# Kernel optimization log

Measured on AMD Instinct MI355X. Metric: run time of the kernel, lower is better.

## Reference

```python
import jax, jax.numpy as jnp
import numpy as np

MODEL_DIM = 1024
NUM_HEADS = 16
CHUNK_LEN = 2048
HEAD_DIM = MODEL_DIM // NUM_HEADS


def setup_inputs() -> dict:
    key = jax.random.key(0)
    ks = jax.random.split(key, 11)
    s = 1.0 / np.sqrt(MODEL_DIM)
    inp = {
        "Q": jax.random.normal(ks[0], (CHUNK_LEN, MODEL_DIM), dtype=jnp.float32),
        "K": jax.random.normal(ks[1], (CHUNK_LEN, MODEL_DIM), dtype=jnp.float32),
        "V": jax.random.normal(ks[2], (CHUNK_LEN, MODEL_DIM), dtype=jnp.float32),
        "Wq": jax.random.normal(ks[3], (MODEL_DIM, MODEL_DIM), dtype=jnp.float32) * s,
        "bq": jax.random.normal(ks[4], (MODEL_DIM,), dtype=jnp.float32) * s,
        "Wk": jax.random.normal(ks[5], (MODEL_DIM, MODEL_DIM), dtype=jnp.float32) * s,
        "bk": jax.random.normal(ks[6], (MODEL_DIM,), dtype=jnp.float32) * s,
        "Wv": jax.random.normal(ks[7], (MODEL_DIM, MODEL_DIM), dtype=jnp.float32) * s,
        "bv": jax.random.normal(ks[8], (MODEL_DIM,), dtype=jnp.float32) * s,
        "Wo": jax.random.normal(ks[9], (MODEL_DIM, MODEL_DIM), dtype=jnp.float32) * s,
        "bo": jax.random.normal(ks[10], (MODEL_DIM,), dtype=jnp.float32) * s,
    }
    return inp


def reference(Q, K, V, Wq, bq, Wk, bk, Wv, bv, Wo, bo):
    S = CHUNK_LEN
    # Linear projections (equinox Linear: y = W @ x + b, vmapped over tokens)
    q = Q @ Wq.T + bq  # [S, D]
    k = K @ Wk.T + bk
    v = V @ Wv.T + bv
    # split heads -> [H, S, hd]
    q = q.reshape(S, NUM_HEADS, HEAD_DIM).transpose(1, 0, 2)
    k = k.reshape(S, NUM_HEADS, HEAD_DIM).transpose(1, 0, 2)
    v = v.reshape(S, NUM_HEADS, HEAD_DIM).transpose(1, 0, 2)
    # scaled dot-product attention with causal mask
    scores = jnp.einsum("hqd,hkd->hqk", q, k) / jnp.sqrt(
        jnp.asarray(HEAD_DIM, dtype=q.dtype)
    )  # [H, S, S]
    causal = jnp.tril(jnp.ones((S, S), dtype=bool))
    scores = jnp.where(causal, scores, -jnp.inf)
    probs = jax.nn.softmax(scores, axis=-1)
    attn = jnp.einsum("hqk,hkd->hqd", probs, v)  # [H, S, hd]
    # combine heads -> [S, D], output projection
    out = attn.transpose(1, 0, 2).reshape(S, MODEL_DIM)
    return out @ Wo.T + bo
```

## Files before the change

kernel.cpp:

```cpp
#include <hip/hip_runtime.h>
#include <hip/hip_bf16.h>
#include <stdint.h>

#define S_LEN  2048
#define DMODEL 1024
#define NHEADS 16
#define HDIM   64
#define CHUNK  7
#define NCHUNK 46

typedef __attribute__((ext_vector_type(8))) _Float16 half8;
typedef __attribute__((ext_vector_type(4))) _Float16 half4;
typedef __attribute__((ext_vector_type(4))) float    f32x4;

struct AttnMap { int base[17]; };

struct CvtArgs {
    const float* src[7];
    _Float16*    dst[7];
    int          n[7];
};

__global__ __launch_bounds__(256) void cvt_kernel(CvtArgs a) {
    const int z = blockIdx.z;
    const float* __restrict__ src = a.src[z];
    _Float16* __restrict__ dst = a.dst[z];
    const int n = a.n[z];
    const int stride = gridDim.x * blockDim.x * 8;
    for (int i = (blockIdx.x * blockDim.x + threadIdx.x) * 8; i < n; i += stride) {
        float4 v0 = *(const float4*)(src + i);
        float4 v1 = *(const float4*)(src + i + 4);
        half8 o;
        o[0] = (_Float16)v0.x; o[1] = (_Float16)v0.y;
        o[2] = (_Float16)v0.z; o[3] = (_Float16)v0.w;
        o[4] = (_Float16)v1.x; o[5] = (_Float16)v1.y;
        o[6] = (_Float16)v1.z; o[7] = (_Float16)v1.w;
        *(half8*)(dst + i) = o;
    }
}

__device__ __forceinline__ void gload16(const _Float16* g, _Float16* l) {
    __builtin_amdgcn_global_load_lds(
        (__attribute__((address_space(1))) void*)const_cast<_Float16*>(g),
        (__attribute__((address_space(3))) void*)l, 16, 0, 0);
}

template<typename OT>
__device__ __forceinline__ void gemm_body(
    const _Float16* __restrict__ A,
    const _Float16* __restrict__ W,
    const float*    __restrict__ bias,
    OT* __restrict__ C, float scale, int bx, int by)
{
    __shared__ _Float16 As[128 * 64];
    __shared__ _Float16 Bs[64 * 64];
    const int tid  = threadIdx.x;
    const int lane = tid & 63, wid = tid >> 6;
    const int row0 = by * 128;
    const int col0 = bx * 64;
    const int wr = wid >> 1, wc = wid & 1;
    const int lr = lane & 15, lg = lane >> 4;
    const int sl = lane & 7;

    f32x4 acc[4][2];
#pragma unroll
    for (int i = 0; i < 4; i++)
#pragma unroll
        for (int j = 0; j < 2; j++) acc[i][j] = (f32x4)(0.0f);

    for (int k0 = 0; k0 < DMODEL; k0 += 64) {
#pragma unroll
        for (int r = 0; r < 4; r++) {
            const int base = r * 256 + wid * 64;
            const int row  = (base + lane) >> 3;
            gload16(A + (size_t)(row0 + row) * DMODEL + k0 + ((sl ^ (row & 7)) * 8),
                    As + (size_t)base * 8);
        }
#pragma unroll
        for (int r = 0; r < 2; r++) {
            const int base = r * 256 + wid * 64;
            const int row  = (base + lane) >> 3;
            gload16(W + (size_t)(col0 + row) * DMODEL + k0 + ((sl ^ (row & 7)) * 8),
                    Bs + (size_t)base * 8);
        }
        __syncthreads();
#pragma unroll
        for (int ks = 0; ks < 2; ks++) {
            half8 af[4], bf[2];
#pragma unroll
            for (int i = 0; i < 4; i++)
                af[i] = *(const half8*)(As + (wr * 64 + i * 16 + lr) * 64 + (((ks * 4 + lg) ^ (lr & 7)) * 8));
#pragma unroll
            for (int j = 0; j < 2; j++)
                bf[j] = *(const half8*)(Bs + (wc * 32 + j * 16 + lr) * 64 + (((ks * 4 + lg) ^ (lr & 7)) * 8));
            __builtin_amdgcn_s_setprio(1);
#pragma unroll
            for (int i = 0; i < 4; i++)
#pragma unroll
                for (int j = 0; j < 2; j++)
                    acc[i][j] = __builtin_amdgcn_mfma_f32_16x16x32_f16(af[i], bf[j], acc[i][j], 0, 0, 0);
            __builtin_amdgcn_s_setprio(0);
        }
        __syncthreads();
    }
#pragma unroll
    for (int i = 0; i < 4; i++)
#pragma unroll
        for (int j = 0; j < 2; j++) {
            const int row = row0 + wr * 64 + i * 16 + lg * 4;
            const int col = col0 + wc * 32 + j * 16 + lr;
            const float b = bias[col];
#pragma unroll
            for (int rj = 0; rj < 4; rj++) {
                float v = (acc[i][j][rj] + b) * scale;
                if constexpr (sizeof(OT) == 2)
                    C[(size_t)(row + rj) * DMODEL + col] = (OT)(_Float16)v;
                else
                    C[(size_t)(row + rj) * DMODEL + col] = v;
            }
        }
}

struct QKVArgs {
    const _Float16* A[3];
    const _Float16* W[3];
    const float*    bias[3];
    _Float16*       C[3];
    float           scale[3];
};

__global__ __launch_bounds__(256) void gemm_qkv(QKVArgs a) {
    const int nper = (int)gridDim.x >> 3;
    const int sid  = ((int)blockIdx.x & 7) * nper + ((int)blockIdx.x >> 3);
    const int z  = sid >> 8;
    const int r  = sid & 255;
    const int by = r >> 4, bx = r & 15;
    gemm_body<_Float16>(a.A[z], a.W[z], a.bias[z], a.C[z], a.scale[z], bx, by);
}

__global__ __launch_bounds__(256) void gemm_out_k(const _Float16* __restrict__ A,
                                                  const _Float16* __restrict__ W,
                                                  const float* __restrict__ bias,
                                                  float* __restrict__ C) {
    const int nper = (int)gridDim.x >> 3;
    const int sid  = ((int)blockIdx.x & 7) * nper + ((int)blockIdx.x >> 3);
    const int by = sid >> 4, bx = sid & 15;
    gemm_body<float>(A, W, bias, C, 1.0f, bx, by);
}

__global__ __launch_bounds__(256) void transpose_v(const _Float16* __restrict__ v,
                                                   _Float16* __restrict__ Vt) {
    __shared__ _Float16 t[64][72];
    const int s0 = blockIdx.x * 64;
    const int h  = blockIdx.y;
    const int tid = threadIdx.x;
#pragma unroll
    for (int r = 0; r < 2; r++) {
        const int g = r * 256 + tid;
        const int sr = g >> 3, c8 = (g & 7) * 8;
        *(half8*)(&t[sr][c8]) = *(const half8*)(v + (size_t)(s0 + sr) * DMODEL + h * HDIM + c8);
    }
    __syncthreads();
#pragma unroll
    for (int r = 0; r < 2; r++) {
        const int g = r * 256 + tid;
        const int d = g >> 3, c8 = (g & 7) * 8;
        half8 o;
#pragma unroll
        for (int j = 0; j < 8; j++) o[j] = t[c8 + j][d];
        *(half8*)(Vt + (size_t)(h * HDIM + d) * S_LEN + s0 + c8) = o;
    }
}

__global__ __launch_bounds__(512, 6) void attn_kernel(
    const _Float16* __restrict__ q,
    const _Float16* __restrict__ k,
    const _Float16* __restrict__ Vt,
    _Float16* __restrict__ Opart,
    float2* __restrict__ ml,
    AttnMap map)
{
    __shared__ _Float16 Kl[2][64 * 64];
    __shared__ _Float16 Vl[2][64 * 64];
    __shared__ _Float16 P[8][16][72];
    const int tid = threadIdx.x, lane = tid & 63, wid = tid >> 6;
    const int x = NCHUNK - 1 - (int)blockIdx.x;
    const int h = blockIdx.y;
    int qt = 0;
    while (map.base[qt + 1] <= x) qt++;
    const int c  = x - map.base[qt];
    const int q0 = qt * 128 + wid * 16;
    const int lr = lane & 15, lg = lane >> 4;
    const int srcb = lg * 20;

    const int r8 = lane >> 3, sl = lane & 7;
    const int ssw = (sl ^ r8) * 8;

    half8 qf[2];
#pragma unroll
    for (int ds = 0; ds < 2; ds++)
        qf[ds] = *(const half8*)(q + (size_t)(q0 + lr) * DMODEL + h * HDIM + ds * 32 + lg * 8);

    float m = -1e30f, lsum = 0.0f;
    f32x4 od[4];
#pragma unroll
    for (int dt = 0; dt < 4; dt++) od[dt] = (f32x4)(0.0f);

    const int T2 = 2 * (qt + 1);
    const int t0 = c * CHUNK;
    const int t1 = (T2 < t0 + CHUNK) ? T2 : (t0 + CHUNK);

    auto stage = [&](int b, int t) {
        const int kb = t * 64;
        gload16(k + (size_t)(kb + wid * 8 + r8) * DMODEL + h * HDIM + ssw,
                &Kl[b][wid * 8 * 64]);
        gload16(Vt + (size_t)(h * HDIM + wid * 8 + r8) * S_LEN + kb + ssw,
                &Vl[b][wid * 8 * 64]);
    };

    int cur = 0;
    stage(0, t0);
    __syncthreads();

    for (int t = t0; t < t1; t++) {
        if (t + 1 < t1) stage(cur ^ 1, t + 1);
        const int k0 = t * 64;
        f32x4 sc[4];
#pragma unroll
        for (int kt = 0; kt < 4; kt++) sc[kt] = (f32x4)(0.0f);
        __builtin_amdgcn_s_setprio(1);
#pragma unroll
        for (int kt = 0; kt < 4; kt++)
#pragma unroll
            for (int ds = 0; ds < 2; ds++) {
                half8 kf = *(const half8*)(&Kl[cur][(kt * 16 + lr) * 64 + (((ds * 4 + lg) ^ (lr & 7)) * 8)]);
                sc[kt] = __builtin_amdgcn_mfma_f32_16x16x32_f16(kf, qf[ds], sc[kt], 0, 0, 0);
            }
        __builtin_amdgcn_s_setprio(0);
        if (k0 + 63 > q0) {
            const int qrow = q0 + lr;
#pragma unroll
            for (int kt = 0; kt < 4; kt++) {
                const int kb2 = k0 + kt * 16 + lg * 4;
#pragma unroll
                for (int r = 0; r < 4; r++)
                    if (kb2 + r > qrow) sc[kt][r] = -1e30f;
            }
        }
        float mk[4];
#pragma unroll
        for (int kt = 0; kt < 4; kt++)
            mk[kt] = fmaxf(fmaxf(sc[kt][0], sc[kt][1]), fmaxf(sc[kt][2], sc[kt][3]));
        float vmax = fmaxf(fmaxf(mk[0], mk[1]), fmaxf(mk[2], mk[3]));
        vmax = fmaxf(vmax, __shfl_xor(vmax, 16));
        vmax = fmaxf(vmax, __shfl_xor(vmax, 32));
        if (!__all(vmax <= m + 8.0f)) {
            const float mnew = fmaxf(m, vmax);
            const float sfac = __expf(m - mnew);
            m = mnew;
            lsum *= sfac;
            float sf[4];
#pragma unroll
            for (int r = 0; r < 4; r++) sf[r] = __shfl(sfac, srcb + r);
#pragma unroll
            for (int dt = 0; dt < 4; dt++)
#pragma unroll
                for (int r = 0; r < 4; r++) od[dt][r] *= sf[r];
        }
        float ps[4];
#pragma unroll
        for (int kt = 0; kt < 4; kt++) {
            float p0 = __expf(sc[kt][0] - m), p1 = __expf(sc[kt][1] - m);
            float p2 = __expf(sc[kt][2] - m), p3 = __expf(sc[kt][3] - m);
            sc[kt][0] = p0; sc[kt][1] = p1; sc[kt][2] = p2; sc[kt][3] = p3;
            ps[kt] = (p0 + p1) + (p2 + p3);
        }
        float psum = (ps[0] + ps[1]) + (ps[2] + ps[3]);
        psum += __shfl_xor(psum, 16);
        psum += __shfl_xor(psum, 32);
        lsum += psum;
#pragma unroll
        for (int kt = 0; kt < 4; kt++) {
            half4 ph;
#pragma unroll
            for (int r = 0; r < 4; r++) ph[r] = (_Float16)sc[kt][r];
            *(half4*)(&P[wid][lr][kt * 16 + lg * 4]) = ph;
        }
        __builtin_amdgcn_s_setprio(1);
#pragma unroll
        for (int ks = 0; ks < 2; ks++) {
            half8 pa = *(const half8*)(&P[wid][lr][ks * 32 + lg * 8]);
#pragma unroll
            for (int dt = 0; dt < 4; dt++) {
                half8 vb = *(const half8*)(&Vl[cur][(dt * 16 + lr) * 64 + (((ks * 4 + lg) ^ (lr & 7)) * 8)]);
                od[dt] = __builtin_amdgcn_mfma_f32_16x16x32_f16(pa, vb, od[dt], 0, 0, 0);
            }
        }
        __builtin_amdgcn_s_setprio(0);
        __syncthreads();
        cur ^= 1;
    }

    const float inv = 1.0f / lsum;
    float invb[4];
#pragma unroll
    for (int r = 0; r < 4; r++) invb[r] = __shfl(inv, srcb + r);
    _Float16* Ob = Opart + ((size_t)h * NCHUNK + x) * 128 * 64;
#pragma unroll
    for (int dt = 0; dt < 4; dt++)
#pragma unroll
        for (int r = 0; r < 4; r++)
            Ob[(size_t)(wid * 16 + lg * 4 + r) * 64 + dt * 16 + lr] = (_Float16)(od[dt][r] * invb[r]);
    if (lane < 16) {
        float2 v; v.x = m; v.y = lsum;
        ml[((size_t)h * NCHUNK + x) * 128 + wid * 16 + lr] = v;
    }
}

__global__ __launch_bounds__(256) void combine_kernel(
    const _Float16* __restrict__ Opart, const float2* __restrict__ ml,
    _Float16* __restrict__ at, AttnMap map)
{
    const int idx = blockIdx.x * 256 + threadIdx.x;
    const int qrow = idx >> 7;
    const int c8 = (idx & 127) * 8;
    const int h = c8 >> 6, d = c8 & 63;
    const int qt = qrow >> 7;
    const int cb = map.base[qt];
    const int nc = map.base[qt + 1] - cb;
    const int lrow = qrow & 127;

    float M = -1e30f, denom = 0.0f;
    float acc[8];
#pragma unroll
    for (int j = 0; j < 8; j++) acc[j] = 0.0f;
    for (int cc = 0; cc < nc; cc++) {
        const size_t ci = (size_t)h * NCHUNK + cb + cc;
        const float2 mlv = ml[ci * 128 + lrow];
        half8 ov = *(const half8*)(Opart + (ci * 128 + lrow) * 64 + d);
        if (mlv.x > M) {
            const float r = __expf(M - mlv.x);
            denom = denom * r + mlv.y;
#pragma unroll
            for (int j = 0; j < 8; j++) acc[j] = acc[j] * r + (float)ov[j] * mlv.y;
            M = mlv.x;
        } else {
            const float w = __expf(mlv.x - M) * mlv.y;
            denom += w;
#pragma unroll
            for (int j = 0; j < 8; j++) acc[j] += (float)ov[j] * w;
        }
    }
    const float inv = 1.0f / denom;
    half8 o;
#pragma unroll
    for (int j = 0; j < 8; j++) o[j] = (_Float16)(acc[j] * inv);
    *(half8*)(at + (size_t)qrow * DMODEL + c8) = o;
}

extern "C" void kernel_launch(void* const* d_in, const int* in_sizes, int n_in,
                              void* d_out, int out_size, void* d_ws, size_t ws_size,
                              hipStream_t stream) {
    const float* Q  = (const float*)d_in[0];
    const float* K  = (const float*)d_in[1];
    const float* V  = (const float*)d_in[2];
    const float* Wq = (const float*)d_in[3];
    const float* bq = (const float*)d_in[4];
    const float* Wk = (const float*)d_in[5];
    const float* bk = (const float*)d_in[6];
    const float* Wv = (const float*)d_in[7];
    const float* bv = (const float*)d_in[8];
    const float* Wo = (const float*)d_in[9];
    const float* bo = (const float*)d_in[10];

    char* w = (char*)d_ws;
    const size_t MB = 1 << 20;
    _Float16* Qh  = (_Float16*)(w + 0 * MB);
    _Float16* Kh  = (_Float16*)(w + 4 * MB);
    _Float16* Vh  = (_Float16*)(w + 8 * MB);
    _Float16* Wqh = (_Float16*)(w + 12 * MB);
    _Float16* Wkh = (_Float16*)(w + 14 * MB);
    _Float16* Wvh = (_Float16*)(w + 16 * MB);
    _Float16* vh  = (_Float16*)(w + 18 * MB);
    _Float16* Woh = (_Float16*)(w + 22 * MB);
    _Float16* qh  = (_Float16*)(w + 24 * MB);
    _Float16* kh  = (_Float16*)(w + 28 * MB);
    _Float16* Vt    = (_Float16*)(w + 0 * MB);
    _Float16* Opart = (_Float16*)(w + 4 * MB);
    float2*   ml    = (float2*)(w + 4 * MB + (size_t)NHEADS * NCHUNK * 128 * 64 * 2);
    _Float16* at    = (_Float16*)(w + 18 * MB);

    const size_t SD = (size_t)S_LEN * DMODEL;
    const size_t WD = (size_t)DMODEL * DMODEL;

    CvtArgs ca;
    ca.src[0] = Q;  ca.dst[0] = Qh;  ca.n[0] = (int)SD;
    ca.src[1] = K;  ca.dst[1] = Kh;  ca.n[1] = (int)SD;
    ca.src[2] = V;  ca.dst[2] = Vh;  ca.n[2] = (int)SD;
    ca.src[3] = Wq; ca.dst[3] = Wqh; ca.n[3] = (int)WD;
    ca.src[4] = Wk; ca.dst[4] = Wkh; ca.n[4] = (int)WD;
    ca.src[5] = Wv; ca.dst[5] = Wvh; ca.n[5] = (int)WD;
    ca.src[6] = Wo; ca.dst[6] = Woh; ca.n[6] = (int)WD;
    cvt_kernel<<<dim3(1024, 1, 7), 256, 0, stream>>>(ca);

    QKVArgs ga;
    ga.A[0] = Qh; ga.W[0] = Wqh; ga.bias[0] = bq; ga.C[0] = qh; ga.scale[0] = 0.125f;
    ga.A[1] = Kh; ga.W[1] = Wkh; ga.bias[1] = bk; ga.C[1] = kh; ga.scale[1] = 1.0f;
    ga.A[2] = Vh; ga.W[2] = Wvh; ga.bias[2] = bv; ga.C[2] = vh; ga.scale[2] = 1.0f;
    gemm_qkv<<<dim3(768), 256, 0, stream>>>(ga);

    transpose_v<<<dim3(32, 16), 256, 0, stream>>>(vh, Vt);

    AttnMap map;
    map.base[0] = 0;
    for (int qt = 0; qt < 16; qt++)
        map.base[qt + 1] = map.base[qt] + (2 * (qt + 1) + CHUNK - 1) / CHUNK;

    attn_kernel<<<dim3(NCHUNK, NHEADS), 512, 0, stream>>>(qh, kh, Vt, Opart, ml, map);
    combine_kernel<<<dim3(1024), 256, 0, stream>>>(Opart, ml, at, map);
    gemm_out_k<<<dim3(256), 256, 0, stream>>>(at, Woh, bo, (float*)d_out);
}
```

Measured before the change: 84.52 us.

## Double-buffer GEMM LDS tiles, halve output-GEMM tile rows, use exp2 softmax

The shared GEMM body now double-buffers its A/B LDS tiles so the next k-slice's global-to-LDS loads are issued before the current slice's MFMAs. It is also templated on tile height: the output projection uses 64-row tiles and twice as many blocks to better fill the CUs. Separately, the Q scale folds in log2(e) so attention and combine can use exp2f instead of __expf. The costs are doubled LDS per block, which may reduce occupancy, and the ml values written by attention are now in base-2 units.

```diff
diff --git a/kernel.cpp b/kernel.cpp
--- a/kernel.cpp
+++ b/kernel.cpp
@@ -8,6 +8,7 @@
 #define HDIM   64
 #define CHUNK  7
 #define NCHUNK 46
+#define LOG2E  1.4426950408889634f
 
 typedef __attribute__((ext_vector_type(8))) _Float16 half8;
 typedef __attribute__((ext_vector_type(4))) _Float16 half4;
@@ -45,69 +46,77 @@
         (__attribute__((address_space(3))) void*)l, 16, 0, 0);
 }
 
-template<typename OT>
+template<int BM, typename OT>
 __device__ __forceinline__ void gemm_body(
     const _Float16* __restrict__ A,
     const _Float16* __restrict__ W,
     const float*    __restrict__ bias,
     OT* __restrict__ C, float scale, int bx, int by)
 {
-    __shared__ _Float16 As[128 * 64];
-    __shared__ _Float16 Bs[64 * 64];
+    constexpr int FI = BM / 32;
+    __shared__ _Float16 As[2][BM * 64];
+    __shared__ _Float16 Bs[2][64 * 64];
     const int tid  = threadIdx.x;
     const int lane = tid & 63, wid = tid >> 6;
-    const int row0 = by * 128;
+    const int row0 = by * BM;
     const int col0 = bx * 64;
     const int wr = wid >> 1, wc = wid & 1;
     const int lr = lane & 15, lg = lane >> 4;
     const int sl = lane & 7;
 
-    f32x4 acc[4][2];
-#pragma unroll
-    for (int i = 0; i < 4; i++)
+    f32x4 acc[FI][2];
+#pragma unroll
+    for (int i = 0; i < FI; i++)
 #pragma unroll
         for (int j = 0; j < 2; j++) acc[i][j] = (f32x4)(0.0f);
 
-    for (int k0 = 0; k0 < DMODEL; k0 += 64) {
-#pragma unroll
-        for (int r = 0; r < 4; r++) {
+    auto stage = [&](int b, int k0) {
+#pragma unroll
+        for (int r = 0; r < BM / 32; r++) {
             const int base = r * 256 + wid * 64;
             const int row  = (base + lane) >> 3;
             gload16(A + (size_t)(row0 + row) * DMODEL + k0 + ((sl ^ (row & 7)) * 8),
-                    As + (size_t)base * 8);
+                    &As[b][(size_t)base * 8]);
         }
 #pragma unroll
         for (int r = 0; r < 2; r++) {
             const int base = r * 256 + wid * 64;
             const int row  = (base + lane) >> 3;
             gload16(W + (size_t)(col0 + row) * DMODEL + k0 + ((sl ^ (row & 7)) * 8),
-                    Bs + (size_t)base * 8);
-        }
-        __syncthreads();
+                    &Bs[b][(size_t)base * 8]);
+        }
+    };
+
+    stage(0, 0);
+    __syncthreads();
+    int cur = 0;
+    for (int t = 0; t < DMODEL / 64; t++) {
+        if (t + 1 < DMODEL / 64) stage(cur ^ 1, (t + 1) * 64);
 #pragma unroll
         for (int ks = 0; ks < 2; ks++) {
-            half8 af[4], bf[2];
-#pragma unroll
-            for (int i = 0; i < 4; i++)
-                af[i] = *(const half8*)(As + (wr * 64 + i * 16 + lr) * 64 + (((ks * 4 + lg) ^ (lr & 7)) * 8));
+            half8 af[FI], bf[2];
+#pragma unroll
+            for (int i = 0; i < FI; i++)
+                af[i] = *(const half8*)(&As[cur][(wr * (BM / 2) + i * 16 + lr) * 64 + (((ks * 4 + lg) ^ (lr & 7)) * 8)]);
 #pragma unroll
             for (int j = 0; j < 2; j++)
-                bf[j] = *(const half8*)(Bs + (wc * 32 + j * 16 + lr) * 64 + (((ks * 4 + lg) ^ (lr & 7)) * 8));
+                bf[j] = *(const half8*)(&Bs[cur][(wc * 32 + j * 16 + lr) * 64 + (((ks * 4 + lg) ^ (lr & 7)) * 8)]);
             __builtin_amdgcn_s_setprio(1);
 #pragma unroll
-            for (int i = 0; i < 4; i++)
+            for (int i = 0; i < FI; i++)
 #pragma unroll
                 for (int j = 0; j < 2; j++)
                     acc[i][j] = __builtin_amdgcn_mfma_f32_16x16x32_f16(af[i], bf[j], acc[i][j], 0, 0, 0);
             __builtin_amdgcn_s_setprio(0);
         }
         __syncthreads();
-    }
-#pragma unroll
-    for (int i = 0; i < 4; i++)
+        cur ^= 1;
+    }
+#pragma unroll
+    for (int i = 0; i < FI; i++)
 #pragma unroll
         for (int j = 0; j < 2; j++) {
-            const int row = row0 + wr * 64 + i * 16 + lg * 4;
+            const int row = row0 + wr * (BM / 2) + i * 16 + lg * 4;
             const int col = col0 + wc * 32 + j * 16 + lr;
             const float b = bias[col];
 #pragma unroll
@@ -135,7 +144,7 @@
     const int z  = sid >> 8;
     const int r  = sid & 255;
     const int by = r >> 4, bx = r & 15;
-    gemm_body<_Float16>(a.A[z], a.W[z], a.bias[z], a.C[z], a.scale[z], bx, by);
+    gemm_body<128, _Float16>(a.A[z], a.W[z], a.bias[z], a.C[z], a.scale[z], bx, by);
 }
 
 __global__ __launch_bounds__(256) void gemm_out_k(const _Float16* __restrict__ A,
@@ -145,7 +154,7 @@
     const int nper = (int)gridDim.x >> 3;
     const int sid  = ((int)blockIdx.x & 7) * nper + ((int)blockIdx.x >> 3);
     const int by = sid >> 4, bx = sid & 15;
-    gemm_body<float>(A, W, bias, C, 1.0f, bx, by);
+    gemm_body<64, float>(A, W, bias, C, 1.0f, bx, by);
 }
 
 __global__ __launch_bounds__(256) void transpose_v(const _Float16* __restrict__ v,
@@ -256,7 +265,7 @@
         vmax = fmaxf(vmax, __shfl_xor(vmax, 32));
         if (!__all(vmax <= m + 8.0f)) {
             const float mnew = fmaxf(m, vmax);
-            const float sfac = __expf(m - mnew);
+            const float sfac = exp2f(m - mnew);
             m = mnew;
             lsum *= sfac;
             float sf[4];
@@ -270,8 +279,8 @@
         float ps[4];
 #pragma unroll
         for (int kt = 0; kt < 4; kt++) {
-            float p0 = __expf(sc[kt][0] - m), p1 = __expf(sc[kt][1] - m);
-            float p2 = __expf(sc[kt][2] - m), p3 = __expf(sc[kt][3] - m);
+            float p0 = exp2f(sc[kt][0] - m), p1 = exp2f(sc[kt][1] - m);
+            float p2 = exp2f(sc[kt][2] - m), p3 = exp2f(sc[kt][3] - m);
             sc[kt][0] = p0; sc[kt][1] = p1; sc[kt][2] = p2; sc[kt][3] = p3;
             ps[kt] = (p0 + p1) + (p2 + p3);
         }
@@ -339,13 +348,13 @@
         const float2 mlv = ml[ci * 128 + lrow];
         half8 ov = *(const half8*)(Opart + (ci * 128 + lrow) * 64 + d);
         if (mlv.x > M) {
-            const float r = __expf(M - mlv.x);
+            const float r = exp2f(M - mlv.x);
             denom = denom * r + mlv.y;
 #pragma unroll
             for (int j = 0; j < 8; j++) acc[j] = acc[j] * r + (float)ov[j] * mlv.y;
             M = mlv.x;
         } else {
-            const float w = __expf(mlv.x - M) * mlv.y;
+            const float w = exp2f(mlv.x - M) * mlv.y;
             denom += w;
 #pragma unroll
             for (int j = 0; j < 8; j++) acc[j] += (float)ov[j] * w;
@@ -404,7 +413,7 @@
     cvt_kernel<<<dim3(1024, 1, 7), 256, 0, stream>>>(ca);
 
     QKVArgs ga;
-    ga.A[0] = Qh; ga.W[0] = Wqh; ga.bias[0] = bq; ga.C[0] = qh; ga.scale[0] = 0.125f;
+    ga.A[0] = Qh; ga.W[0] = Wqh; ga.bias[0] = bq; ga.C[0] = qh; ga.scale[0] = 0.125f * LOG2E;
     ga.A[1] = Kh; ga.W[1] = Wkh; ga.bias[1] = bk; ga.C[1] = kh; ga.scale[1] = 1.0f;
     ga.A[2] = Vh; ga.W[2] = Wvh; ga.bias[2] = bv; ga.C[2] = vh; ga.scale[2] = 1.0f;
     gemm_qkv<<<dim3(768), 256, 0, stream>>>(ga);
@@ -418,5 +427,5 @@
 
     attn_kernel<<<dim3(NCHUNK, NHEADS), 512, 0, stream>>>(qh, kh, Vt, Opart, ml, map);
     combine_kernel<<<dim3(1024), 256, 0, stream>>>(Opart, ml, at, map);
-    gemm_out_k<<<dim3(256), 256, 0, stream>>>(at, Woh, bo, (float*)d_out);
-}
+    gemm_out_k<<<dim3(512), 256, 0, stream>>>(at, Woh, bo, (float*)d_out);
+}
```

Measured after the change: 83.70 us. Within noise of the previous version (-1.0%).
